# Kernel optimization log

Hardware: AMD Instinct MI355X
Metric: run time of the kernel (lower is better)

The kernel has to match this reference:

```python
import jax, jax.numpy as jnp
import numpy as np
from jax import lax

N_CLASS = 21          # VOC: 20 foreground + background
SCORE_THRESH = 0.05   # 'evaluate' preset
NMS_THRESH = 0.3


def loc2bbox(src_bbox, loc):
    # src_bbox, loc: [N, 4] in (y1, x1, y2, x2) / (dy, dx, dh, dw)
    h = src_bbox[:, 2] - src_bbox[:, 0]
    w = src_bbox[:, 3] - src_bbox[:, 1]
    cy = src_bbox[:, 0] + 0.5 * h
    cx = src_bbox[:, 1] + 0.5 * w
    dy, dx, dh, dw = loc[:, 0], loc[:, 1], loc[:, 2], loc[:, 3]
    ncy = dy * h + cy
    ncx = dx * w + cx
    nh = jnp.exp(dh) * h
    nw = jnp.exp(dw) * w
    return jnp.stack([ncy - 0.5 * nh, ncx - 0.5 * nw,
                      ncy + 0.5 * nh, ncx + 0.5 * nw], axis=1)


def pairwise_iou(boxes):
    # boxes: [R, 4] (y1, x1, y2, x2) -> [R, R]
    area = (boxes[:, 2] - boxes[:, 0]) * (boxes[:, 3] - boxes[:, 1])
    ty1 = jnp.maximum(boxes[:, None, 0], boxes[None, :, 0])
    tx1 = jnp.maximum(boxes[:, None, 1], boxes[None, :, 1])
    ty2 = jnp.minimum(boxes[:, None, 2], boxes[None, :, 2])
    tx2 = jnp.minimum(boxes[:, None, 3], boxes[None, :, 3])
    inter = jnp.clip(ty2 - ty1, 0) * jnp.clip(tx2 - tx1, 0)
    union = area[:, None] + area[None, :] - inter
    return inter / jnp.maximum(union, 1e-10)


def nms_keep(boxes, scores):
    # boxes [R,4], scores [R] for one class. Returns bool keep mask [R]
    # (score-thresholded + greedy NMS), fixed shape (mask instead of gather).
    R = boxes.shape[0]
    valid = scores > SCORE_THRESH
    order = jnp.argsort(-scores)
    b = boxes[order]
    v = valid[order]
    suppress = pairwise_iou(b) > NMS_THRESH  # [R, R]
    idx = jnp.arange(R)

    def body(i, keep):
        sup_by_earlier = jnp.any(keep & suppress[:, i] & (idx < i))
        return keep.at[i].set(v[i] & ~sup_by_earlier)

    keep_sorted = lax.fori_loop(0, R, body, jnp.zeros((R,), bool))
    return jnp.zeros((R,), bool).at[order].set(keep_sorted)


def setup_inputs() -> dict:
    key = jax.random.key(0)
    k1, k2, k3, k4 = jax.random.split(key, 4)
    R = 2000
    size_h, size_w = 600, 800
    roi_cls_loc = jax.random.normal(k1, (R, N_CLASS * 4), jnp.float32)
    roi_scores = jax.random.normal(k2, (R, N_CLASS), jnp.float32)
    # valid (y1, x1, y2, x2) rois inside the image
    yx = jax.random.uniform(k3, (R, 2), jnp.float32) * jnp.array([size_h - 32.0, size_w - 32.0])
    hw = 16.0 + jax.random.uniform(k4, (R, 2), jnp.float32) * 128.0
    rois = jnp.concatenate([yx, yx + hw], axis=1)
    return {"roi_cls_loc": roi_cls_loc, "roi_scores": roi_scores,
            "rois": rois, "size_h": size_h, "size_w": size_w}


def reference(roi_cls_loc, roi_scores, rois, size_h, size_w):
    R = rois.shape[0]
    mean = jnp.tile(jnp.asarray([0.0, 0.0, 0.0, 0.0], roi_cls_loc.dtype), N_CLASS)
    std = jnp.tile(jnp.asarray([0.1, 0.1, 0.2, 0.2], roi_cls_loc.dtype), N_CLASS)
    loc = roi_cls_loc * std + mean                      # [R, 4*C]
    loc = loc.reshape(R * N_CLASS, 4)
    src = jnp.broadcast_to(rois[:, None, :], (R, N_CLASS, 4)).reshape(R * N_CLASS, 4)
    box = loc2bbox(src, loc).reshape(R, N_CLASS, 4)
    # clamp y coords (0,2) to [0, H], x coords (1,3) to [0, W]
    y = jnp.clip(box[..., 0::2], 0.0, float(size_h))
    x = jnp.clip(box[..., 1::2], 0.0, float(size_w))
    box = jnp.stack([y[..., 0], x[..., 0], y[..., 1], x[..., 1]], axis=-1)
    prob = jax.nn.softmax(roi_scores, axis=1)           # [R, C]
    # foreground classes only (skip background class 0)
    cls_box = jnp.transpose(box[:, 1:, :], (1, 0, 2))   # [C-1, R, 4]
    cls_prob = prob[:, 1:].T                            # [C-1, R]
    keep = jax.vmap(nms_keep)(lax.stop_gradient(cls_box),
                              lax.stop_gradient(cls_prob))  # [C-1, R] bool
    kept = keep.astype(box.dtype)[..., None]
    # fixed-shape detections: per-class boxes + score, zeroed where suppressed
    out = jnp.concatenate([cls_box * kept, cls_prob[..., None] * kept], axis=-1)
    return out  # [C-1, R, 5]
```

## Files before the change

### kernel.cpp

```cpp
#include <hip/hip_runtime.h>
#include <math.h>

#define NCLS 21
#define NCO 20
#define SUB 8
#define TPB 256
#define STH 1024
#define RCAP 2048
#define RMAX 2000
#define LDSW 7680
#define SCORE_THRESH 0.05f

typedef unsigned long long u64;
typedef unsigned int u32;
typedef unsigned short u16;

#define IOU_MID (20132661.0 / 67108864.0)

__device__ __forceinline__ u64 readlane64(u64 v, int l) {
    u32 lo = (u32)__builtin_amdgcn_readlane((int)(u32)v, l);
    u32 hi = (u32)__builtin_amdgcn_readlane((int)(u32)(v >> 32), l);
    return ((u64)hi << 32) | lo;
}
__device__ __forceinline__ float readlanef(float v, int l) {
    return __uint_as_float((u32)__builtin_amdgcn_readlane((int)__float_as_uint(v), l));
}
__device__ __forceinline__ u64 shflxor64(u64 v, int m) {
    u32 lo = (u32)__shfl_xor((int)(u32)v, m, 64);
    u32 hi = (u32)__shfl_xor((int)(u32)(v >> 32), m, 64);
    return ((u64)hi << 32) | lo;
}

__device__ __forceinline__ int coff(int ic, int nw) {
    return ((ic * nw - ((ic * (ic - 1)) >> 1)) << 6);
}

__device__ __forceinline__ void decode_box(
    const float* __restrict__ rois, const float* __restrict__ loc,
    int r, int cls, float sh, float sw,
    float& by1, float& bx1, float& by2, float& bx2)
{
    float4 rb = *(const float4*)(rois + r * 4);
    float y1 = rb.x, x1 = rb.y, y2 = rb.z, x2 = rb.w;
    float h = y2 - y1, w = x2 - x1;
    float cy = y1 + 0.5f * h, cx = x1 + 0.5f * w;
    float4 l4 = *(const float4*)(loc + r * (NCLS * 4) + cls * 4);
    float dy = l4.x * 0.1f, dx = l4.y * 0.1f;
    float dh = l4.z * 0.2f, dw = l4.w * 0.2f;
    float ncy = dy * h + cy, ncx = dx * w + cx;
    float nh = expf(dh) * h, nw = expf(dw) * w;
    by1 = fminf(fmaxf(ncy - 0.5f * nh, 0.f), sh);
    bx1 = fminf(fmaxf(ncx - 0.5f * nw, 0.f), sw);
    by2 = fminf(fmaxf(ncy + 0.5f * nh, 0.f), sh);
    bx2 = fminf(fmaxf(ncx + 0.5f * nw, 0.f), sw);
}

__device__ __forceinline__ float softmax_p(
    const float* __restrict__ scores, int r, int cls)
{
    const float* srow = scores + r * NCLS;
    float s[NCLS];
    float4 a0 = *(const float4*)(srow);
    float4 a1 = *(const float4*)(srow + 4);
    float4 a2 = *(const float4*)(srow + 8);
    float4 a3 = *(const float4*)(srow + 12);
    float4 a4 = *(const float4*)(srow + 16);
    s[0]=a0.x; s[1]=a0.y; s[2]=a0.z; s[3]=a0.w;
    s[4]=a1.x; s[5]=a1.y; s[6]=a1.z; s[7]=a1.w;
    s[8]=a2.x; s[9]=a2.y; s[10]=a2.z; s[11]=a2.w;
    s[12]=a3.x; s[13]=a3.y; s[14]=a3.z; s[15]=a3.w;
    s[16]=a4.x; s[17]=a4.y; s[18]=a4.z; s[19]=a4.w;
    s[20]=srow[20];
    float m = -INFINITY;
#pragma unroll
    for (int k = 0; k < NCLS; ++k) m = fmaxf(m, s[k]);
    float sum = 0.f, ec = 0.f;
#pragma unroll
    for (int k = 0; k < NCLS; ++k) {
        float e = expf(s[k] - m);
        sum += e;
        if (k == cls) ec = e;
    }
    return ec / sum;
}

__global__ __launch_bounds__(STH) void sort_kernel(
    const float* __restrict__ scores, u64* __restrict__ ord,
    int* __restrict__ nvv, int R)
{
    __shared__ u64 vkey[RCAP];
    __shared__ int cnt;
    const int t = threadIdx.x;
    const int c = blockIdx.x;
    const int lane = t & 63;
    if (t == 0) cnt = 0;
    __syncthreads();

    for (int r = t; r < R; r += STH) {
        float p = softmax_p(scores, r, c + 1);
        bool valid = (p > SCORE_THRESH);
        u64 key = ((u64)(~__float_as_uint(p)) << 32) | (u32)r;
        u64 bal = __ballot(valid);
        if (bal) {
            int nb = (int)__popcll(bal);
            int base = 0;
            if (lane == 0) base = atomicAdd(&cnt, nb);
            base = __shfl(base, 0, 64);
            if (valid)
                vkey[base + (int)__popcll(bal & ((1ull << lane) - 1ull))] = key;
        }
    }
    __syncthreads();
    const int nv = cnt;
    if (t == 0) nvv[c] = nv;

    for (int ibase = 0; ibase < nv; ibase += STH) {
        int i = ibase + t;
        if (i < nv) {
            u64 kj = vkey[i];
            int rank = 0;
#pragma unroll 4
            for (int j = 0; j < nv; ++j)
                rank += (vkey[j] < kj);
            ord[((size_t)c << 11) + rank] = kj;
        }
    }
}

__global__ __launch_bounds__(TPB) void mask_kernel(
    const float* __restrict__ loc, const float* __restrict__ rois,
    const int* __restrict__ ph, const int* __restrict__ pw,
    const u64* __restrict__ ord, const int* __restrict__ nvv,
    u64* __restrict__ M, int R)
{
    __shared__ float4 pb[RCAP];
    __shared__ float ar[RCAP];
    const int t = threadIdx.x;
    const int c = blockIdx.x >> 3;
    const int s = blockIdx.x & 7;
    const int nv = nvv[c];
    const int nw = (nv + 63) >> 6;
    const float sh = (float)(*ph), sw = (float)(*pw);

    for (int i = t; i < nv; i += TPB) {
        u64 key = ord[((size_t)c << 11) + i];
        int r = (int)(u32)key;
        float a0, a1, a2, a3;
        decode_box(rois, loc, r, c + 1, sh, sw, a0, a1, a2, a3);
        pb[i] = make_float4(a0, a1, a2, a3);
        ar[i] = (a2 - a0) * (a3 - a1);
    }
    __syncthreads();

    const int lane = t & 63;
    const int wid = (s << 2) | (t >> 6);
    const int ntasks = nw * (nw + 1) / 2;
    u64* Mc = M + ((size_t)c << 16);
    for (int task = wid; task < ntasks; task += SUB * 4) {
        int ic = 0, rm = task;
        while (rm >= nw - ic) { rm -= nw - ic; ++ic; }
        int v = ic + rm;
        int i = (ic << 6) + lane;
        float4 a = pb[i];
        float iarea = ar[i];
        float4 rj = pb[(v << 6) + lane];
        float ja_l = ar[(v << 6) + lane];
        int jcnt = min(64, nv - (v << 6));
        u64 m = 0;
        for (int jj = 0; jj < jcnt; ++jj) {
            float jy1 = readlanef(rj.x, jj);
            float jx1 = readlanef(rj.y, jj);
            float jy2 = readlanef(rj.z, jj);
            float jx2 = readlanef(rj.w, jj);
            float ja  = readlanef(ja_l, jj);
            float ty1 = fmaxf(a.x, jy1);
            float tx1 = fmaxf(a.y, jx1);
            float ty2 = fminf(a.z, jy2);
            float tx2 = fminf(a.w, jx2);
            float inter = fmaxf(ty2 - ty1, 0.f) * fmaxf(tx2 - tx1, 0.f);
            float uni = fmaxf(iarea + ja - inter, 1e-10f);
            if ((double)inter > IOU_MID * (double)uni) m |= 1ull << jj;
        }
        if (v == ic) m &= (lane < 63) ? (~0ull << (lane + 1)) : 0ull;
        int W = nw - ic;
        if (i < nv) Mc[coff(ic, nw) + lane * W + (v - ic)] = m;
    }
}

__global__ __launch_bounds__(TPB) void resolveout_kernel(
    const float* __restrict__ loc, const float* __restrict__ rois,
    const int* __restrict__ ph, const int* __restrict__ pw,
    const u64* __restrict__ ord, const int* __restrict__ nvv,
    const u64* __restrict__ M, float* __restrict__ out, int R)
{
    __shared__ u64 mlds[LDSW];
    __shared__ u64 keptw[32];
    const int t = threadIdx.x;
    const int c = blockIdx.x >> 3;
    const int s = blockIdx.x & 7;
    const int nv = nvv[c];
    const int nw = (nv + 63) >> 6;
    const u64* Mc = M + ((size_t)c << 16);
    const int S = coff(nw, nw);
    const bool lds_ok = (S <= LDSW);
    if (t < 32) keptw[t] = 0;

    if (lds_ok) {
        for (int base = 0; base < S; base += 2048) {
            u64 v[8];
#pragma unroll
            for (int j = 0; j < 8; ++j) {
                int k = base + (j << 8) + t;
                v[j] = (k < S) ? Mc[k] : 0ull;
            }
#pragma unroll
            for (int j = 0; j < 8; ++j) {
                int k = base + (j << 8) + t;
                if (k < S) mlds[k] = v[j];
            }
        }
    }
    __syncthreads();

    if (t < 64) {
        const int lane = t;
        auto core = [&](const auto* B) {
            u64 remreg = 0;
            for (int w = 0; w < nw; ++w) {
                const int W = nw - w;
                const int cb = coff(w, nw);
                int i = (w << 6) + lane;
                u64 cw = (i < nv) ? B[cb + lane * W] : 0ull;
                int remn = nv - (w << 6);
                u64 vb = (remn >= 64) ? ~0ull : ((1ull << remn) - 1ull);
                u64 cand = vb & ~readlane64(remreg, w);
                u64 X = cand;
                if (X) {
                    for (int it = 0; it < 64; ++it) {
                        u64 contrib = ((X >> lane) & 1ull) ? cw : 0ull;
#pragma unroll
                        for (int d = 1; d < 64; d <<= 1)
                            contrib |= shflxor64(contrib, d);
                        bool keep = ((cand >> lane) & 1ull) &&
                                    !((contrib >> lane) & 1ull);
                        u64 Xn = __ballot(keep);
                        if (Xn == X) break;
                        X = Xn;
                    }
                    if (lane == 0) keptw[w] = X;
                    bool lact = (lane > w) && (lane < nw);
                    u64 km = X, acc = 0;
                    while (km) {
                        int bs[8];
#pragma unroll
                        for (int g = 0; g < 8; ++g) {
                            bs[g] = km ? (__ffsll(km) - 1) : -1;
                            if (km) km &= km - 1;
                        }
                        u64 tmp[8];
#pragma unroll
                        for (int g = 0; g < 8; ++g)
                            tmp[g] = (bs[g] >= 0 && lact)
                                ? B[cb + bs[g] * W + (lane - w)] : 0ull;
#pragma unroll
                        for (int g = 0; g < 8; ++g) acc |= tmp[g];
                    }
                    if (lact) remreg |= acc;
                }
            }
        };
        if (lds_ok) core(mlds); else core(Mc);
    }
    __syncthreads();

    const int chunk = (R + 7) >> 3;
    const int r0 = s * chunk;
    const int r1 = min(R, r0 + chunk);
    float* slice = out + (size_t)c * R * 5;
    for (int k = r0 * 5 + t; k < r1 * 5; k += TPB) slice[k] = 0.f;
    __syncthreads();

    const float sh = (float)(*ph), sw = (float)(*pw);
    for (int i = t; i < nv; i += TPB) {
        if ((keptw[i >> 6] >> (i & 63)) & 1ull) {
            u64 key = ord[((size_t)c << 11) + i];
            int r = (int)(u32)key;
            if (r >= r0 && r < r1) {
                float v0, v1, v2, v3;
                decode_box(rois, loc, r, c + 1, sh, sw, v0, v1, v2, v3);
                float* p = slice + (size_t)r * 5;
                p[0] = v0; p[1] = v1; p[2] = v2; p[3] = v3;
                p[4] = __uint_as_float(~(u32)(key >> 32));
            }
        }
    }
}

#define NTH 1024
__global__ __launch_bounds__(NTH) void fused_kernel(
    const float* __restrict__ loc, const float* __restrict__ scores,
    const float* __restrict__ rois, const int* __restrict__ ph,
    const int* __restrict__ pw, float* __restrict__ out, int R)
{
    __shared__ u64 vkey[RMAX];
    __shared__ float2 p1[RMAX], p2[RMAX];
    __shared__ u64 chunk[64 * 33];
    __shared__ u64 rem[32];
    __shared__ int cnt;

    const int t = threadIdx.x;
    const int lane = t & 63;
    const int c = blockIdx.x + 1;
    const float sh = (float)(*ph), sw = (float)(*pw);

    if (t == 0) cnt = 0;
    if (t < 32) rem[t] = 0;
    __syncthreads();

    for (int r = t; r < R; r += NTH) {
        float p = softmax_p(scores, r, c);
        if (p > SCORE_THRESH) {
            int j = atomicAdd(&cnt, 1);
            vkey[j] = ((u64)(~__float_as_uint(p)) << 32) | (u32)r;
        }
    }
    __syncthreads();
    const int nv = cnt;
    const int nw = (nv + 63) >> 6;

    u64 kk0 = 0, kk1 = 0;
    int r0 = 0, r1 = 0;
    bool in0 = (t < nv), in1 = (t + NTH < nv);
    if (in0) kk0 = vkey[t];
    if (in1) kk1 = vkey[t + NTH];
#pragma unroll 8
    for (int i = 0; i < nv; ++i) {
        u64 k = vkey[i];
        r0 += (k < kk0);
        r1 += (k < kk1);
    }
    __syncthreads();

    for (int u = 0; u < 2; ++u) {
        bool act = u ? in1 : in0;
        if (act) {
            u64 kk = u ? kk1 : kk0;
            int rank = u ? r1 : r0;
            int r = (int)(kk & 0xffffffffu);
            float b0, b1, b2, b3;
            decode_box(rois, loc, r, c, sh, sw, b0, b1, b2, b3);
            vkey[rank] = kk;
            p1[rank] = make_float2(b0, b1);
            p2[rank] = make_float2(b2, b3);
        }
    }
    __syncthreads();

    for (int w = 0; w < nw; ++w) {
        int nwr = nw - w;
        u64 remw = rem[w];
        for (int task = t; task < (nwr << 6); task += NTH) {
            int vr = task >> 6, il = task & 63;
            int i = (w << 6) + il;
            u64 m = 0;
            if (i < nv && !((remw >> il) & 1ull)) {
                int v = w + vr;
                u64 rv = rem[v];
                if (~rv != 0ull) {
                    float2 a1 = p1[i], a2 = p2[i];
                    float iarea = (a2.x - a1.x) * (a2.y - a1.y);
                    int j0 = v << 6;
                    int jhi = min(64, nv - j0);
#pragma unroll 4
                    for (int jj = 0; jj < jhi; ++jj) {
                        float2 b1 = p1[j0 + jj], b2 = p2[j0 + jj];
                        float ty1 = fmaxf(a1.x, b1.x);
                        float tx1 = fmaxf(a1.y, b1.y);
                        float ty2 = fminf(a2.x, b2.x);
                        float tx2 = fminf(a2.y, b2.y);
                        float inter = fmaxf(ty2 - ty1, 0.f) * fmaxf(tx2 - tx1, 0.f);
                        float jarea = (b2.x - b1.x) * (b2.y - b1.y);
                        float uni = fmaxf(iarea + jarea - inter, 1e-10f);
                        if ((double)inter > IOU_MID * (double)uni) m |= 1ull << jj;
                    }
                    if (vr == 0)
                        m &= (il < 63) ? (~0ull << (il + 1)) : 0ull;
                }
            }
            chunk[il * 33 + vr] = m;
        }
        __syncthreads();

        u64 cand = chunk[lane * 33];
        u64 cur = rem[w];
        int remn = nv - (w << 6);
        u64 vb = (remn >= 64) ? ~0ull : ((1ull << remn) - 1ull);
        u64 avail = vb & ~cur;
        u64 kept = 0;
        while (avail) {
            int bb = __ffsll(avail) - 1;
            kept |= 1ull << bb;
            cur |= __shfl(cand, bb, 64);
            avail &= ~(cur | (1ull << bb));
        }
        int vr = t & 31, pg = t >> 5;
        if (vr >= 1 && vr < nwr) {
            u64 acc = 0, km = kept;
            int n = 0;
            while (km) {
                int bb = __ffsll(km) - 1;
                km &= km - 1;
                if ((n & 31) == pg) acc |= chunk[bb * 33 + vr];
                ++n;
            }
            if (acc) atomicOr(&rem[w + vr], acc);
        }
        if (t == 0) rem[w] = cur;
        __syncthreads();
    }

    u16* inv = (u16*)chunk;
    for (int r = t; r < R; r += NTH) inv[r] = 0xffffu;
    __syncthreads();
    for (int i = t; i < nv; i += NTH)
        if (!((rem[i >> 6] >> (i & 63)) & 1ull))
            inv[(int)(vkey[i] & 0xffffffffu)] = (u16)i;
    __syncthreads();
    float* slice = out + (size_t)(c - 1) * R * 5;
    for (int r = t; r < R; r += NTH) {
        int i = inv[r];
        float v0 = 0.f, v1 = 0.f, v2 = 0.f, v3 = 0.f, v4 = 0.f;
        if (i != 0xffff) {
            float2 a1 = p1[i], a2 = p2[i];
            v0 = a1.x; v1 = a1.y; v2 = a2.x; v3 = a2.y;
            v4 = __uint_as_float(~(u32)(vkey[i] >> 32));
        }
        float* p = slice + (size_t)r * 5;
        p[0] = v0; p[1] = v1; p[2] = v2; p[3] = v3; p[4] = v4;
    }
}

extern "C" void kernel_launch(void* const* d_in, const int* in_sizes, int n_in,
                              void* d_out, int out_size, void* d_ws, size_t ws_size,
                              hipStream_t stream) {
    const float* loc    = (const float*)d_in[0];
    const float* scores = (const float*)d_in[1];
    const float* rois   = (const float*)d_in[2];
    const int*   ph     = (const int*)d_in[3];
    const int*   pw     = (const int*)d_in[4];
    float* out = (float*)d_out;
    int R = in_sizes[2] / 4;

    size_t needM   = (size_t)NCO * RCAP * 32 * 8;
    size_t needOrd = (size_t)NCO * RCAP * 8;
    size_t need    = needM + needOrd + 128;

    if (R <= RCAP && ws_size >= need) {
        char* w   = (char*)d_ws;
        u64* M    = (u64*)w;
        u64* ordp = (u64*)(w + needM);
        int* nvv  = (int*)(w + needM + needOrd);
        sort_kernel<<<NCO, STH, 0, stream>>>(scores, ordp, nvv, R);
        mask_kernel<<<NCO * SUB, TPB, 0, stream>>>(loc, rois, ph, pw, ordp, nvv,
                                                   M, R);
        resolveout_kernel<<<NCO * SUB, TPB, 0, stream>>>(loc, rois, ph, pw,
                                                         ordp, nvv, M, out, R);
    } else if (R <= RMAX) {
        fused_kernel<<<NCO, NTH, 0, stream>>>(loc, scores, rois, ph, pw, out, R);
    }
}
```

Baseline: 128.5 us.

## Fuse score sort into mask kernel with redundant per-subblock rank sort

Merges the separate sort kernel into the IoU mask kernel: each of the 8 sub-blocks per class now recomputes the softmax filtering and rank sort itself in LDS, then builds boxes straight from the sorted keys instead of reading them back from global memory. The rank sort is restructured so each thread holds up to 8 keys in registers and scans the key array once. This removes one kernel launch and the global round trip of the sorted order. In exchange, the softmax and O(nv^2) sort work is done 8 times redundantly, with 256 threads per block instead of 1024.

```diff
diff --git a/kernel.cpp b/kernel.cpp
--- a/kernel.cpp
+++ b/kernel.cpp
@@ -5,7 +5,6 @@
 #define NCO 20
 #define SUB 8
 #define TPB 256
-#define STH 1024
 #define RCAP 2048
 #define RMAX 2000
 #define LDSW 7680
@@ -84,19 +83,25 @@
     return ec / sum;
 }
 
-__global__ __launch_bounds__(STH) void sort_kernel(
-    const float* __restrict__ scores, u64* __restrict__ ord,
-    int* __restrict__ nvv, int R)
+__global__ __launch_bounds__(TPB) void sortmask_kernel(
+    const float* __restrict__ loc, const float* __restrict__ scores,
+    const float* __restrict__ rois, const int* __restrict__ ph,
+    const int* __restrict__ pw, u64* __restrict__ ord,
+    int* __restrict__ nvv, u64* __restrict__ M, int R)
 {
     __shared__ u64 vkey[RCAP];
+    __shared__ float4 pb[RCAP];
+    __shared__ float ar[RCAP];
     __shared__ int cnt;
     const int t = threadIdx.x;
-    const int c = blockIdx.x;
+    const int c = blockIdx.x >> 3;
+    const int s = blockIdx.x & 7;
     const int lane = t & 63;
+    const float sh = (float)(*ph), sw = (float)(*pw);
     if (t == 0) cnt = 0;
     __syncthreads();
 
-    for (int r = t; r < R; r += STH) {
+    for (int r = t; r < R; r += TPB) {
         float p = softmax_p(scores, r, c + 1);
         bool valid = (p > SCORE_THRESH);
         u64 key = ((u64)(~__float_as_uint(p)) << 32) | (u32)r;
@@ -112,47 +117,61 @@
     }
     __syncthreads();
     const int nv = cnt;
-    if (t == 0) nvv[c] = nv;
-
-    for (int ibase = 0; ibase < nv; ibase += STH) {
-        int i = ibase + t;
-        if (i < nv) {
-            u64 kj = vkey[i];
-            int rank = 0;
+    const int nw = (nv + 63) >> 6;
+
+    u64 k0=~0ull,k1=~0ull,k2=~0ull,k3=~0ull,k4=~0ull,k5=~0ull,k6=~0ull,k7=~0ull;
+    if (t < nv)            k0 = vkey[t];
+    if (t + 256 < nv)      k1 = vkey[t + 256];
+    if (t + 512 < nv)      k2 = vkey[t + 512];
+    if (t + 768 < nv)      k3 = vkey[t + 768];
+    int r0=0,r1=0,r2=0,r3=0,r4=0,r5=0,r6=0,r7=0;
+    if (nv <= 1024) {
 #pragma unroll 4
-            for (int j = 0; j < nv; ++j)
-                rank += (vkey[j] < kj);
-            ord[((size_t)c << 11) + rank] = kj;
-        }
-    }
-}
-
-__global__ __launch_bounds__(TPB) void mask_kernel(
-    const float* __restrict__ loc, const float* __restrict__ rois,
-    const int* __restrict__ ph, const int* __restrict__ pw,
-    const u64* __restrict__ ord, const int* __restrict__ nvv,
-    u64* __restrict__ M, int R)
-{
-    __shared__ float4 pb[RCAP];
-    __shared__ float ar[RCAP];
-    const int t = threadIdx.x;
-    const int c = blockIdx.x >> 3;
-    const int s = blockIdx.x & 7;
-    const int nv = nvv[c];
-    const int nw = (nv + 63) >> 6;
-    const float sh = (float)(*ph), sw = (float)(*pw);
+        for (int j = 0; j < nv; ++j) {
+            u64 kj = vkey[j];
+            r0 += (kj < k0); r1 += (kj < k1);
+            r2 += (kj < k2); r3 += (kj < k3);
+        }
+    } else {
+        if (t + 1024 < nv) k4 = vkey[t + 1024];
+        if (t + 1280 < nv) k5 = vkey[t + 1280];
+        if (t + 1536 < nv) k6 = vkey[t + 1536];
+        if (t + 1792 < nv) k7 = vkey[t + 1792];
+#pragma unroll 2
+        for (int j = 0; j < nv; ++j) {
+            u64 kj = vkey[j];
+            r0 += (kj < k0); r1 += (kj < k1); r2 += (kj < k2); r3 += (kj < k3);
+            r4 += (kj < k4); r5 += (kj < k5); r6 += (kj < k6); r7 += (kj < k7);
+        }
+    }
+    __syncthreads();
+    if (t < nv)            vkey[r0] = k0;
+    if (t + 256 < nv)      vkey[r1] = k1;
+    if (t + 512 < nv)      vkey[r2] = k2;
+    if (t + 768 < nv)      vkey[r3] = k3;
+    if (nv > 1024) {
+        if (t + 1024 < nv) vkey[r4] = k4;
+        if (t + 1280 < nv) vkey[r5] = k5;
+        if (t + 1536 < nv) vkey[r6] = k6;
+        if (t + 1792 < nv) vkey[r7] = k7;
+    }
+    __syncthreads();
 
     for (int i = t; i < nv; i += TPB) {
-        u64 key = ord[((size_t)c << 11) + i];
+        u64 key = vkey[i];
         int r = (int)(u32)key;
         float a0, a1, a2, a3;
         decode_box(rois, loc, r, c + 1, sh, sw, a0, a1, a2, a3);
         pb[i] = make_float4(a0, a1, a2, a3);
         ar[i] = (a2 - a0) * (a3 - a1);
     }
-    __syncthreads();
-
-    const int lane = t & 63;
+    if (s == 0) {
+        for (int i = t; i < nv; i += TPB)
+            ord[((size_t)c << 11) + i] = vkey[i];
+        if (t == 0) nvv[c] = nv;
+    }
+    __syncthreads();
+
     const int wid = (s << 2) | (t >> 6);
     const int ntasks = nw * (nw + 1) / 2;
     u64* Mc = M + ((size_t)c << 16);
@@ -460,9 +479,8 @@
         u64* M    = (u64*)w;
         u64* ordp = (u64*)(w + needM);
         int* nvv  = (int*)(w + needM + needOrd);
-        sort_kernel<<<NCO, STH, 0, stream>>>(scores, ordp, nvv, R);
-        mask_kernel<<<NCO * SUB, TPB, 0, stream>>>(loc, rois, ph, pw, ordp, nvv,
-                                                   M, R);
+        sortmask_kernel<<<NCO * SUB, TPB, 0, stream>>>(loc, scores, rois, ph, pw,
+                                                       ordp, nvv, M, R);
         resolveout_kernel<<<NCO * SUB, TPB, 0, stream>>>(loc, rois, ph, pw,
                                                          ordp, nvv, M, out, R);
     } else if (R <= RMAX) {
```

Result: slower. 139.3 us (+8.4%).

## Split per-class sort into parallel keygen and rank kernels, precompute decoded boxes

Applied to the files above, without the earlier changes.

The single-block-per-class sort kernel is replaced by a keygen kernel spread over 8 blocks per class and a rank kernel that also spreads the rank-counting over 8 blocks per class. The rank kernel reads keys as pairs and decodes boxes and areas directly into sorted order, so the mask kernel only loads precomputed boxes instead of re-decoding them in every one of its 8 blocks per class. The mask kernel also moves to 512 threads. This trades one more kernel launch and extra global round-trips for much more parallelism in the sort stage, which previously ran on only 20 blocks.

```diff
diff --git a/kernel.cpp b/kernel.cpp
--- a/kernel.cpp
+++ b/kernel.cpp
@@ -5,7 +5,6 @@
 #define NCO 20
 #define SUB 8
 #define TPB 256
-#define STH 1024
 #define RCAP 2048
 #define RMAX 2000
 #define LDSW 7680
@@ -84,19 +83,21 @@
     return ec / sum;
 }
 
-__global__ __launch_bounds__(STH) void sort_kernel(
-    const float* __restrict__ scores, u64* __restrict__ ord,
-    int* __restrict__ nvv, int R)
-{
-    __shared__ u64 vkey[RCAP];
+__global__ __launch_bounds__(256) void keygen_kernel(
+    const float* __restrict__ scores, u64* __restrict__ ukey,
+    int* __restrict__ cntA, int R)
+{
+    __shared__ u64 lkey[256];
     __shared__ int cnt;
     const int t = threadIdx.x;
-    const int c = blockIdx.x;
+    const int c = blockIdx.x >> 3;
+    const int s = blockIdx.x & 7;
     const int lane = t & 63;
     if (t == 0) cnt = 0;
     __syncthreads();
-
-    for (int r = t; r < R; r += STH) {
+    const int rpb = (R + 7) >> 3;
+    const int r0 = s * rpb, r1 = min(R, r0 + rpb);
+    for (int r = r0 + t; r < r1; r += 256) {
         float p = softmax_p(scores, r, c + 1);
         bool valid = (p > SCORE_THRESH);
         u64 key = ((u64)(~__float_as_uint(p)) << 32) | (u32)r;
@@ -107,56 +108,87 @@
             if (lane == 0) base = atomicAdd(&cnt, nb);
             base = __shfl(base, 0, 64);
             if (valid)
-                vkey[base + (int)__popcll(bal & ((1ull << lane) - 1ull))] = key;
-        }
-    }
-    __syncthreads();
-    const int nv = cnt;
-    if (t == 0) nvv[c] = nv;
-
-    for (int ibase = 0; ibase < nv; ibase += STH) {
-        int i = ibase + t;
-        if (i < nv) {
-            u64 kj = vkey[i];
-            int rank = 0;
-#pragma unroll 4
-            for (int j = 0; j < nv; ++j)
-                rank += (vkey[j] < kj);
-            ord[((size_t)c << 11) + rank] = kj;
-        }
-    }
-}
-
-__global__ __launch_bounds__(TPB) void mask_kernel(
+                lkey[base + (int)__popcll(bal & ((1ull << lane) - 1ull))] = key;
+        }
+    }
+    __syncthreads();
+    const int n = cnt;
+    if (t == 0) cntA[(c << 3) | s] = n;
+    for (int j = t; j < n; j += 256)
+        ukey[((size_t)c << 11) + (s << 8) + j] = lkey[j];
+}
+
+__global__ __launch_bounds__(512) void rank_kernel(
     const float* __restrict__ loc, const float* __restrict__ rois,
     const int* __restrict__ ph, const int* __restrict__ pw,
-    const u64* __restrict__ ord, const int* __restrict__ nvv,
-    u64* __restrict__ M, int R)
+    const u64* __restrict__ ukey, const int* __restrict__ cntA,
+    u64* __restrict__ ord, int* __restrict__ nvv,
+    float4* __restrict__ pbG, float* __restrict__ arG, int R)
+{
+    __shared__ __align__(16) u64 vkey[RCAP + 2];
+    const int t = threadIdx.x;
+    const int c = blockIdx.x >> 3;
+    const int s = blockIdx.x & 7;
+    const int wv = t >> 6, lane = t & 63;
+    int nv = 0, bseg = 0, nseg = 0;
+#pragma unroll
+    for (int k = 0; k < 8; ++k) {
+        int ck = cntA[(c << 3) | k];
+        if (k < wv) bseg += ck;
+        if (k == wv) nseg = ck;
+        nv += ck;
+    }
+    for (int j = lane; j < nseg; j += 64)
+        vkey[bseg + j] = ukey[((size_t)c << 11) + (wv << 8) + j];
+    if (t == 0) vkey[nv] = ~0ull;
+    __syncthreads();
+
+    const int sl = (nv + 7) >> 3;
+    const int i0 = s * sl;
+    const int nmy = max(0, min(nv - i0, sl));
+    if (t < nmy) {
+        u64 kk = vkey[i0 + t];
+        int rank = 0;
+        const ulonglong2* vk2 = (const ulonglong2*)vkey;
+        const int nj2 = (nv + 1) >> 1;
+#pragma unroll 8
+        for (int j = 0; j < nj2; ++j) {
+            ulonglong2 kj = vk2[j];
+            rank += (int)(kj.x < kk) + (int)(kj.y < kk);
+        }
+        const float sh = (float)(*ph), sw = (float)(*pw);
+        int r = (int)(u32)kk;
+        float b0, b1, b2, b3;
+        decode_box(rois, loc, r, c + 1, sh, sw, b0, b1, b2, b3);
+        ord[((size_t)c << 11) + rank] = kk;
+        pbG[((size_t)c << 11) + rank] = make_float4(b0, b1, b2, b3);
+        arG[((size_t)c << 11) + rank] = (b2 - b0) * (b3 - b1);
+    }
+    if (t == 0 && s == 0) nvv[c] = nv;
+}
+
+__global__ __launch_bounds__(512) void maskp_kernel(
+    const float4* __restrict__ pbG, const float* __restrict__ arG,
+    const int* __restrict__ nvv, u64* __restrict__ M)
 {
     __shared__ float4 pb[RCAP];
     __shared__ float ar[RCAP];
     const int t = threadIdx.x;
     const int c = blockIdx.x >> 3;
     const int s = blockIdx.x & 7;
+    const int lane = t & 63;
     const int nv = nvv[c];
     const int nw = (nv + 63) >> 6;
-    const float sh = (float)(*ph), sw = (float)(*pw);
-
-    for (int i = t; i < nv; i += TPB) {
-        u64 key = ord[((size_t)c << 11) + i];
-        int r = (int)(u32)key;
-        float a0, a1, a2, a3;
-        decode_box(rois, loc, r, c + 1, sh, sw, a0, a1, a2, a3);
-        pb[i] = make_float4(a0, a1, a2, a3);
-        ar[i] = (a2 - a0) * (a3 - a1);
-    }
-    __syncthreads();
-
-    const int lane = t & 63;
-    const int wid = (s << 2) | (t >> 6);
+    for (int i = t; i < nv; i += 512) {
+        pb[i] = pbG[((size_t)c << 11) + i];
+        ar[i] = arG[((size_t)c << 11) + i];
+    }
+    __syncthreads();
+
+    const int wid = (s << 3) | (t >> 6);
     const int ntasks = nw * (nw + 1) / 2;
     u64* Mc = M + ((size_t)c << 16);
-    for (int task = wid; task < ntasks; task += SUB * 4) {
+    for (int task = wid; task < ntasks; task += SUB * 8) {
         int ic = 0, rm = task;
         while (rm >= nw - ic) { rm -= nw - ic; ++ic; }
         int v = ic + rm;
@@ -451,18 +483,26 @@
     float* out = (float*)d_out;
     int R = in_sizes[2] / 4;
 
-    size_t needM   = (size_t)NCO * RCAP * 32 * 8;
-    size_t needOrd = (size_t)NCO * RCAP * 8;
-    size_t need    = needM + needOrd + 128;
+    size_t needM    = (size_t)NCO * RCAP * 32 * 8;
+    size_t needOrd  = (size_t)NCO * RCAP * 8;
+    size_t needUkey = (size_t)NCO * RCAP * 8;
+    size_t needPbG  = (size_t)NCO * RCAP * 16;
+    size_t needArG  = (size_t)NCO * RCAP * 4;
+    size_t need     = needM + needOrd + needUkey + needPbG + needArG + 2048;
 
     if (R <= RCAP && ws_size >= need) {
-        char* w   = (char*)d_ws;
-        u64* M    = (u64*)w;
-        u64* ordp = (u64*)(w + needM);
-        int* nvv  = (int*)(w + needM + needOrd);
-        sort_kernel<<<NCO, STH, 0, stream>>>(scores, ordp, nvv, R);
-        mask_kernel<<<NCO * SUB, TPB, 0, stream>>>(loc, rois, ph, pw, ordp, nvv,
-                                                   M, R);
+        char* w     = (char*)d_ws;
+        u64* M      = (u64*)w;                               w += needM;
+        u64* ordp   = (u64*)w;                               w += needOrd;
+        u64* ukey   = (u64*)w;                               w += needUkey;
+        float4* pbG = (float4*)w;                            w += needPbG;
+        float* arG  = (float*)w;                             w += needArG;
+        int* cntA   = (int*)w;                               w += 1024;
+        int* nvv    = (int*)w;
+        keygen_kernel<<<NCO * SUB, 256, 0, stream>>>(scores, ukey, cntA, R);
+        rank_kernel<<<NCO * SUB, 512, 0, stream>>>(loc, rois, ph, pw, ukey,
+                                                   cntA, ordp, nvv, pbG, arG, R);
+        maskp_kernel<<<NCO * SUB, 512, 0, stream>>>(pbG, arG, nvv, M);
         resolveout_kernel<<<NCO * SUB, TPB, 0, stream>>>(loc, rois, ph, pw,
                                                          ordp, nvv, M, out, R);
     } else if (R <= RMAX) {
```

Measured after the change: 116.8 us. 1.1x faster.
